# Performance work log

Hardware: AMD Instinct MI355X
Metric: run time of the kernel (lower is better)

The kernel has to match this reference:

```python
import jax, jax.numpy as jnp
import numpy as np

B, L, C = 4, 2048, 1024
H = 16
D = C // H  # head_dim = 64


def _rope(t, cos, sin):
    # t: [B, H, L, D]; cos/sin: [L, D//2] broadcast to [1, 1, L, D//2]
    te = t[..., ::2]
    to = t[..., 1::2]
    c = cos[None, None]
    s = sin[None, None]
    re = te * c - to * s
    ro = te * s + to * c
    # interleave even/odd back: [..., D//2, 2] -> [..., D]
    return jnp.stack([re, ro], axis=-1).reshape(t.shape)


def setup_inputs() -> dict:
    key = jax.random.key(0)
    ks = jax.random.split(key, 5)
    x = jax.random.normal(ks[0], (B, L, C), dtype=jnp.float32)
    # rotary phases: theta_i = 10000^(-2i/D), angles = pos * theta
    inv_freq = 1.0 / (10000.0 ** (np.arange(0, D, 2, dtype=np.float32) / D))
    ang = np.arange(L, dtype=np.float32)[:, None] * inv_freq[None, :]  # [L, D//2]
    cos = jnp.asarray(np.cos(ang))
    sin = jnp.asarray(np.sin(ang))
    w_qkv = jax.random.normal(ks[1], (3 * C, C), dtype=jnp.float32) * (C ** -0.5)
    w_proj = jax.random.normal(ks[2], (C, C), dtype=jnp.float32) * (C ** -0.5)
    b_proj = jnp.zeros((C,), dtype=jnp.float32)
    return {"x": x, "cos": cos, "sin": sin, "w_qkv": w_qkv, "w_proj": w_proj, "b_proj": b_proj}


def reference(x, cos, sin, w_qkv, w_proj, b_proj):
    Bx, Lx, Cx = x.shape
    # QKV projection (torch Linear: y = x @ W.T), then split heads
    qkv = jnp.einsum("blc,fc->blf", x, w_qkv)  # [B, L, 3C]
    qkv = qkv.reshape(Bx, Lx, 3, H, D).transpose(2, 0, 3, 1, 4)  # [3, B, H, L, D]
    q, k, v = qkv[0], qkv[1], qkv[2]
    q = _rope(q, cos, sin)
    k = _rope(k, cos, sin)
    # scaled dot-product attention, non-causal
    scale = D ** -0.5
    scores = jnp.einsum("bhqd,bhkd->bhqk", q, k) * scale
    attn = jax.nn.softmax(scores, axis=-1)
    o = jnp.einsum("bhqk,bhkd->bhqd", attn, v)  # [B, H, L, D]
    o = o.transpose(0, 2, 1, 3).reshape(Bx, Lx, Cx)
    return jnp.einsum("blc,fc->blf", o, w_proj) + b_proj
```

## Files before the change

kernel.cpp:

```cpp
#include <hip/hip_runtime.h>
#include <hip/hip_bf16.h>
#include <cstdint>


typedef unsigned short u16;
typedef __attribute__((ext_vector_type(8))) short bf16x8;
typedef __attribute__((ext_vector_type(4))) float f32x4;
typedef __attribute__((ext_vector_type(2))) unsigned int u32x2;

#define GLD16(g, l)                                                            \
  __builtin_amdgcn_global_load_lds(                                            \
      (const __attribute__((address_space(1))) void*)(g),                      \
      (__attribute__((address_space(3))) void*)(l), 16, 0, 0)

static __device__ __forceinline__ u16 f32_bf16(float f) {
  union { float f; unsigned u; } v; v.f = f;
  unsigned r = v.u + 0x7FFFu + ((v.u >> 16) & 1u);
  return (u16)(r >> 16);
}
static __device__ __forceinline__ float bf16_f32(u16 h) {
  union { unsigned u; float f; } v; v.u = ((unsigned)h) << 16;
  return v.f;
}
static __device__ __forceinline__ unsigned pack_rne(float a, float b) {
  union { float f; unsigned u; } x, y; x.f = a; y.f = b;
  unsigned ua = x.u + 0x7FFFu + ((x.u >> 16) & 1u);
  unsigned ub = y.u + 0x7FFFu + ((y.u >> 16) & 1u);
  return (ua >> 16) | (ub & 0xFFFF0000u);
}
static __device__ __forceinline__ unsigned pack_bf16_hw(float a, float b) {
  float2 t; t.x = a; t.y = b;
  __hip_bfloat162 h = __float22bfloat162_rn(t);
  union { __hip_bfloat162 h; unsigned u; } c; c.h = h;
  return c.u;
}
static __device__ __forceinline__ bf16x8 mk_pf(unsigned a, unsigned b,
                                               unsigned c, unsigned d) {
  union { unsigned u[4]; bf16x8 v; } t;
  t.u[0] = a; t.u[1] = b; t.u[2] = c; t.u[3] = d;
  return t.v;
}

__global__ __launch_bounds__(256) void convert_all(
    const void* __restrict__ x, const void* __restrict__ wq,
    const void* __restrict__ wp, const void* __restrict__ cs,
    const void* __restrict__ sn, const void* __restrict__ bs,
    u16* __restrict__ xb, u16* __restrict__ wqb, u16* __restrict__ wpb,
    u16* __restrict__ cb, u16* __restrict__ sb, u16* __restrict__ bb) {
  const unsigned f32mode = (((const unsigned*)cs)[0] == 0x3F800000u);
  int blk = blockIdx.x;
  const void* src; u16* dst; int i0, n4;
  if (blk < 8192)       { src = x;  dst = xb;  i0 = blk;         n4 = 2097152; }
  else if (blk < 11264) { src = wq; dst = wqb; i0 = blk - 8192;  n4 = 786432; }
  else if (blk < 12288) { src = wp; dst = wpb; i0 = blk - 11264; n4 = 262144; }
  else if (blk < 12352) { src = cs; dst = cb;  i0 = blk - 12288; n4 = 16384; }
  else if (blk < 12416) { src = sn; dst = sb;  i0 = blk - 12352; n4 = 16384; }
  else                  { src = bs; dst = bb;  i0 = blk - 12416; n4 = 256; }
  int i = i0 * 256 + threadIdx.x;
  if (i >= n4) return;
  if (f32mode) {
    float4 v = ((const float4*)src)[i];
    uint2 o;
    o.x = pack_rne(v.x, v.y);
    o.y = pack_rne(v.z, v.w);
    ((uint2*)dst)[i] = o;
  } else {
    ((uint2*)dst)[i] = ((const uint2*)src)[i];
  }
}

static __device__ __forceinline__ void gemm_mainloop(
    const u16* __restrict__ A, const u16* __restrict__ Bm, int K,
    int m0, int n0, u16* As, u16* Bs, f32x4 acc[4][4]) {
  const int tid  = threadIdx.x;
  const int lane = tid & 63;
  const int wave = tid >> 6;
  const int n16  = lane & 15;
  const int quad = lane >> 4;
  const int wm = (wave >> 1) * 64;
  const int wn = (wave & 1) * 64;
  const u16* ag = A  + (size_t)(m0 + wave * 16 + (lane >> 2)) * K + (lane & 3) * 8;
  const u16* bg = Bm + (size_t)(n0 + wave * 16 + (lane >> 2)) * K + (lane & 3) * 8;
  u16* al = As + wave * (16 * 32);
  u16* bl = Bs + wave * (16 * 32);
  for (int kt = 0; kt < K; kt += 32) {
    GLD16(ag + kt, al);
    GLD16(ag + (size_t)64 * K + kt, al + 64 * 32);
    GLD16(bg + kt, bl);
    GLD16(bg + (size_t)64 * K + kt, bl + 64 * 32);
    __syncthreads();
    bf16x8 af[4], bf[4];
#pragma unroll
    for (int i = 0; i < 4; i++)
      af[i] = *(const bf16x8*)(As + (wm + i * 16 + n16) * 32 + quad * 8);
#pragma unroll
    for (int j = 0; j < 4; j++)
      bf[j] = *(const bf16x8*)(Bs + (wn + j * 16 + n16) * 32 + quad * 8);
#pragma unroll
    for (int i = 0; i < 4; i++)
#pragma unroll
      for (int j = 0; j < 4; j++)
        acc[i][j] = __builtin_amdgcn_mfma_f32_16x16x32_bf16(af[i], bf[j], acc[i][j], 0, 0, 0);
    __syncthreads();
  }
}

__global__ __launch_bounds__(256) void gemm_qkv(
    const u16* __restrict__ x, const u16* __restrict__ w,
    u16* __restrict__ q_ws, u16* __restrict__ k_ws, u16* __restrict__ vt_ws) {
  __shared__ u16 As[128 * 32];
  __shared__ u16 Bs[128 * 32];
  f32x4 acc[4][4];
#pragma unroll
  for (int i = 0; i < 4; i++)
#pragma unroll
    for (int j = 0; j < 4; j++) acc[i][j] = (f32x4){0.f, 0.f, 0.f, 0.f};
  const int m0 = blockIdx.y * 128;
  const int n0 = blockIdx.x * 128;
  gemm_mainloop(x, w, 1024, m0, n0, As, Bs, acc);
  const int lane = threadIdx.x & 63, wave = threadIdx.x >> 6;
  const int n16 = lane & 15, quad = lane >> 4;
  const int wm = (wave >> 1) * 64, wn = (wave & 1) * 64;
#pragma unroll
  for (int i = 0; i < 4; i++)
#pragma unroll
    for (int j = 0; j < 4; j++) {
      int f = n0 + wn + j * 16 + n16;
      int which = f >> 10;
      int rem = f & 1023;
      int h = rem >> 6, d = rem & 63;
      int l0 = m0 + wm + i * 16 + quad * 4;
      int b = l0 >> 11, l = l0 & 2047;
      if (which == 2) {
        uint2 o;
        o.x = pack_rne(acc[i][j][0], acc[i][j][1]);
        o.y = pack_rne(acc[i][j][2], acc[i][j][3]);
        size_t idx = (((size_t)b * 16 + h) * 64 + d) * 2048 + l;
        *(uint2*)(vt_ws + idx) = o;
      } else {
        u16* dst = (which == 0) ? q_ws : k_ws;
        size_t base = (((size_t)b * 16 + h) * 2048 + l) * 64 + d;
#pragma unroll
        for (int r = 0; r < 4; r++)
          dst[base + (size_t)r * 64] = f32_bf16(acc[i][j][r]);
      }
    }
}

#define NP_ROPE 4194304
__global__ __launch_bounds__(256) void rope_qk(
    u16* __restrict__ q, u16* __restrict__ k,
    const u16* __restrict__ cosp, const u16* __restrict__ sinp) {
  int idx = blockIdx.x * 256 + threadIdx.x;
  bool isq = (idx < NP_ROPE);
  u16* t = isq ? q : k;
  float sc = isq ? 0.18033688011112042f : 1.0f;
  int p = isq ? idx : idx - NP_ROPE;
  int l = (p >> 5) & 2047;
  int i = p & 31;
  unsigned v = ((unsigned*)t)[p];
  float te = bf16_f32((u16)(v & 0xFFFFu));
  float to = bf16_f32((u16)(v >> 16));
  float c = bf16_f32(cosp[l * 32 + i]);
  float s = bf16_f32(sinp[l * 32 + i]);
  ((unsigned*)t)[p] = pack_rne((te * c - to * s) * sc, (te * s + to * c) * sc);
}

__global__ __launch_bounds__(256, 4) void flash_attn(
    const u16* __restrict__ q_ws, const u16* __restrict__ k_ws,
    const u16* __restrict__ vt_ws, u16* __restrict__ o_ws) {
  __shared__ u16 Ks[2][64 * 64];
  __shared__ u16 Vs[2][64 * 64];
  const int bh = blockIdx.x & 63;
  const int q0 = (blockIdx.x >> 6) * 128;
  const int b = bh >> 4, h = bh & 15;
  const int tid = threadIdx.x, lane = tid & 63, wave = tid >> 6;
  const int n16 = lane & 15, quad = lane >> 4;
  const int x7 = n16 & 7;
  const int pn16 = (n16 & 3) | ((n16 & 4) << 1) | ((n16 & 8) >> 1);
  const int px7 = pn16 & 7;
  const size_t hoff = (size_t)bh * (2048 * 64);

  bf16x8 qf[2][2];
#pragma unroll
  for (int qb = 0; qb < 2; qb++) {
    const u16* qrow = q_ws + hoff + (size_t)(q0 + wave * 32 + qb * 16 + n16) * 64;
    qf[qb][0] = *(const bf16x8*)(qrow + quad * 8);
    qf[qb][1] = *(const bf16x8*)(qrow + 32 + quad * 8);
  }

  f32x4 oacc[2][4];
  f32x4 lq[2];
#pragma unroll
  for (int qb = 0; qb < 2; qb++) {
    lq[qb] = (f32x4){0.f, 0.f, 0.f, 0.f};
#pragma unroll
    for (int s = 0; s < 4; s++) oacc[qb][s] = (f32x4){0.f, 0.f, 0.f, 0.f};
  }

  const int srow = wave * 8 + (lane >> 3);
  const int sw = (lane & 7) ^ ((lane >> 3) & 7);
  const u16* kg = k_ws + hoff + (size_t)srow * 64 + sw * 8;
  const u16* vg = vt_ws + hoff + (size_t)srow * 2048 + sw * 8;
  const int loff = wave * 8 * 64;

  GLD16(kg, &Ks[0][loff]);
  GLD16(kg + 32 * 64, &Ks[0][loff + 32 * 64]);
  GLD16(vg, &Vs[0][loff]);
  GLD16(vg + (size_t)32 * 2048, &Vs[0][loff + 32 * 64]);

  for (int kt = 0; kt < 2048; kt += 64) {
    const int buf = (kt >> 6) & 1;
    __syncthreads();
    if (kt + 64 < 2048) {
      const u16* kgn = kg + (size_t)(kt + 64) * 64;
      const u16* vgn = vg + (kt + 64);
      GLD16(kgn, &Ks[buf ^ 1][loff]);
      GLD16(kgn + 32 * 64, &Ks[buf ^ 1][loff + 32 * 64]);
      GLD16(vgn, &Vs[buf ^ 1][loff]);
      GLD16(vgn + (size_t)32 * 2048, &Vs[buf ^ 1][loff + 32 * 64]);
    }
    const u16* ks = Ks[buf];
    const u16* vs = Vs[buf];

    unsigned pxk[2][4], pyk[2][4];
#pragma unroll
    for (int sub = 0; sub < 4; sub++) {
      const u16* krow = ks + (sub * 16 + pn16) * 64;
      bf16x8 kf0 = *(const bf16x8*)(krow + (quad ^ px7) * 8);
      bf16x8 kf1 = *(const bf16x8*)(krow + ((quad + 4) ^ px7) * 8);
#pragma unroll
      for (int qb = 0; qb < 2; qb++) {
        f32x4 z = (f32x4){0.f, 0.f, 0.f, 0.f};
        z = __builtin_amdgcn_mfma_f32_16x16x32_bf16(kf0, qf[qb][0], z, 0, 0, 0);
        z = __builtin_amdgcn_mfma_f32_16x16x32_bf16(kf1, qf[qb][1], z, 0, 0, 0);
        f32x4 p;
#pragma unroll
        for (int r = 0; r < 4; r++) p[r] = __builtin_amdgcn_exp2f(z[r]);
        lq[qb] += p;
        pxk[qb][sub] = pack_bf16_hw(p[0], p[1]);
        pyk[qb][sub] = pack_bf16_hw(p[2], p[3]);
      }
    }

    bf16x8 pf[2][2];
#pragma unroll
    for (int qb = 0; qb < 2; qb++) {
      u32x2 r0 = __builtin_amdgcn_permlane32_swap(pxk[qb][0], pxk[qb][1], false, false);
      u32x2 r1 = __builtin_amdgcn_permlane32_swap(pyk[qb][0], pyk[qb][1], false, false);
      u32x2 r2 = __builtin_amdgcn_permlane32_swap(pxk[qb][2], pxk[qb][3], false, false);
      u32x2 r3 = __builtin_amdgcn_permlane32_swap(pyk[qb][2], pyk[qb][3], false, false);
      pf[qb][0] = mk_pf(r0.x, r1.x, r0.y, r1.y);
      pf[qb][1] = mk_pf(r2.x, r3.x, r2.y, r3.y);
    }

#pragma unroll
    for (int sd = 0; sd < 4; sd++) {
      const u16* vrow = vs + (sd * 16 + n16) * 64;
      bf16x8 vf0 = *(const bf16x8*)(vrow + (quad ^ x7) * 8);
      bf16x8 vf1 = *(const bf16x8*)(vrow + ((quad + 4) ^ x7) * 8);
#pragma unroll
      for (int qb = 0; qb < 2; qb++) {
        oacc[qb][sd] = __builtin_amdgcn_mfma_f32_16x16x32_bf16(pf[qb][0], vf0, oacc[qb][sd], 0, 0, 0);
        oacc[qb][sd] = __builtin_amdgcn_mfma_f32_16x16x32_bf16(pf[qb][1], vf1, oacc[qb][sd], 0, 0, 0);
      }
    }
  }

#pragma unroll
  for (int qb = 0; qb < 2; qb++) {
    float l = lq[qb][0] + lq[qb][1] + lq[qb][2] + lq[qb][3];
    l += __shfl_xor(l, 16, 64);
    l += __shfl_xor(l, 32, 64);
    float linv = 1.0f / l;
#pragma unroll
    for (int r = 0; r < 4; r++) {
      float lr = __shfl(linv, quad * 4 + r, 64);
      int row = q0 + wave * 32 + qb * 16 + quad * 4 + r;
      size_t base = ((size_t)b * 2048 + row) * 1024 + h * 64;
#pragma unroll
      for (int sd = 0; sd < 4; sd++)
        o_ws[base + sd * 16 + n16] = f32_bf16(oacc[qb][sd][r] * lr);
    }
  }
}

__global__ __launch_bounds__(256) void gemm_proj(
    const u16* __restrict__ o, const u16* __restrict__ w,
    const u16* __restrict__ bias, float* __restrict__ out) {
  __shared__ u16 As[128 * 32];
  __shared__ u16 Bs[128 * 32];
  f32x4 acc[4][4];
#pragma unroll
  for (int i = 0; i < 4; i++)
#pragma unroll
    for (int j = 0; j < 4; j++) acc[i][j] = (f32x4){0.f, 0.f, 0.f, 0.f};
  const int m0 = blockIdx.y * 128;
  const int n0 = blockIdx.x * 128;
  gemm_mainloop(o, w, 1024, m0, n0, As, Bs, acc);
  const int lane = threadIdx.x & 63, wave = threadIdx.x >> 6;
  const int n16 = lane & 15, quad = lane >> 4;
  const int wm = (wave >> 1) * 64, wn = (wave & 1) * 64;
#pragma unroll
  for (int i = 0; i < 4; i++)
#pragma unroll
    for (int j = 0; j < 4; j++) {
      int f = n0 + wn + j * 16 + n16;
      float bf = bf16_f32(bias[f]);
#pragma unroll
      for (int r = 0; r < 4; r++) {
        int m = m0 + wm + i * 16 + quad * 4 + r;
        out[(size_t)m * 1024 + f] = acc[i][j][r] + bf;
      }
    }
}

extern "C" void kernel_launch(void* const* d_in, const int* in_sizes, int n_in,
                              void* d_out, int out_size, void* d_ws, size_t ws_size,
                              hipStream_t stream) {
  float* out = (float*)d_out;

  u16* ws = (u16*)d_ws;
  u16* xb     = ws;
  u16* wqkvb  = ws + 8388608;
  u16* wprojb = ws + 11534336;
  u16* cosb   = ws + 12582912;
  u16* sinb   = ws + 12648448;
  u16* biasb  = ws + 12713984;
  u16* qb     = ws + 12715008;
  u16* kb     = ws + 21103616;
  u16* vtb    = ws + 29492224;
  u16* ob     = xb;

  convert_all<<<12417, 256, 0, stream>>>(
      d_in[0], d_in[3], d_in[4], d_in[1], d_in[2], d_in[5],
      xb, wqkvb, wprojb, cosb, sinb, biasb);

  gemm_qkv<<<dim3(24, 64), 256, 0, stream>>>(xb, wqkvb, qb, kb, vtb);
  rope_qk<<<32768, 256, 0, stream>>>(qb, kb, cosb, sinb);
  flash_attn<<<1024, 256, 0, stream>>>(qb, kb, vtb, ob);
  gemm_proj<<<dim3(8, 64), 256, 0, stream>>>(ob, wprojb, biasb, out);
}
```

Baseline: 288.0 us.

## Software-pipeline PV MFMAs one tile behind QK and add setprio around MFMA

Defers the P·V matrix multiply of each key tile into the next loop iteration, keeping the packed P fragments and V fragments in registers so the PV MFMAs overlap with the next tile's QK MFMAs and exp. A final drain after the loop handles the last tile. It also wraps the MFMA groups in s_setprio so waves issuing matrix ops get scheduling priority. This adds register pressure (V fragments held across the barrier), which may reduce occupancy.

```diff
diff --git a/kernel.cpp b/kernel.cpp
--- a/kernel.cpp
+++ b/kernel.cpp
@@ -209,6 +209,9 @@
   GLD16(vg, &Vs[0][loff]);
   GLD16(vg + (size_t)32 * 2048, &Vs[0][loff + 32 * 64]);
 
+  bf16x8 pfp[2][2];
+  bf16x8 vfp[4][2];
+
   for (int kt = 0; kt < 2048; kt += 64) {
     const int buf = (kt >> 6) & 1;
     __syncthreads();
@@ -232,8 +235,10 @@
 #pragma unroll
       for (int qb = 0; qb < 2; qb++) {
         f32x4 z = (f32x4){0.f, 0.f, 0.f, 0.f};
+        __builtin_amdgcn_s_setprio(1);
         z = __builtin_amdgcn_mfma_f32_16x16x32_bf16(kf0, qf[qb][0], z, 0, 0, 0);
         z = __builtin_amdgcn_mfma_f32_16x16x32_bf16(kf1, qf[qb][1], z, 0, 0, 0);
+        __builtin_amdgcn_s_setprio(0);
         f32x4 p;
 #pragma unroll
         for (int r = 0; r < 4; r++) p[r] = __builtin_amdgcn_exp2f(z[r]);
@@ -243,29 +248,45 @@
       }
     }
 
-    bf16x8 pf[2][2];
+    if (kt) {
+      __builtin_amdgcn_s_setprio(1);
+#pragma unroll
+      for (int sd = 0; sd < 4; sd++)
+#pragma unroll
+        for (int qb = 0; qb < 2; qb++) {
+          oacc[qb][sd] = __builtin_amdgcn_mfma_f32_16x16x32_bf16(pfp[qb][0], vfp[sd][0], oacc[qb][sd], 0, 0, 0);
+          oacc[qb][sd] = __builtin_amdgcn_mfma_f32_16x16x32_bf16(pfp[qb][1], vfp[sd][1], oacc[qb][sd], 0, 0, 0);
+        }
+      __builtin_amdgcn_s_setprio(0);
+    }
+
 #pragma unroll
     for (int qb = 0; qb < 2; qb++) {
       u32x2 r0 = __builtin_amdgcn_permlane32_swap(pxk[qb][0], pxk[qb][1], false, false);
       u32x2 r1 = __builtin_amdgcn_permlane32_swap(pyk[qb][0], pyk[qb][1], false, false);
       u32x2 r2 = __builtin_amdgcn_permlane32_swap(pxk[qb][2], pxk[qb][3], false, false);
       u32x2 r3 = __builtin_amdgcn_permlane32_swap(pyk[qb][2], pyk[qb][3], false, false);
-      pf[qb][0] = mk_pf(r0.x, r1.x, r0.y, r1.y);
-      pf[qb][1] = mk_pf(r2.x, r3.x, r2.y, r3.y);
+      pfp[qb][0] = mk_pf(r0.x, r1.x, r0.y, r1.y);
+      pfp[qb][1] = mk_pf(r2.x, r3.x, r2.y, r3.y);
     }
 
 #pragma unroll
     for (int sd = 0; sd < 4; sd++) {
       const u16* vrow = vs + (sd * 16 + n16) * 64;
-      bf16x8 vf0 = *(const bf16x8*)(vrow + (quad ^ x7) * 8);
-      bf16x8 vf1 = *(const bf16x8*)(vrow + ((quad + 4) ^ x7) * 8);
-#pragma unroll
-      for (int qb = 0; qb < 2; qb++) {
-        oacc[qb][sd] = __builtin_amdgcn_mfma_f32_16x16x32_bf16(pf[qb][0], vf0, oacc[qb][sd], 0, 0, 0);
-        oacc[qb][sd] = __builtin_amdgcn_mfma_f32_16x16x32_bf16(pf[qb][1], vf1, oacc[qb][sd], 0, 0, 0);
-      }
-    }
-  }
+      vfp[sd][0] = *(const bf16x8*)(vrow + (quad ^ x7) * 8);
+      vfp[sd][1] = *(const bf16x8*)(vrow + ((quad + 4) ^ x7) * 8);
+    }
+  }
+
+  __builtin_amdgcn_s_setprio(1);
+#pragma unroll
+  for (int sd = 0; sd < 4; sd++)
+#pragma unroll
+    for (int qb = 0; qb < 2; qb++) {
+      oacc[qb][sd] = __builtin_amdgcn_mfma_f32_16x16x32_bf16(pfp[qb][0], vfp[sd][0], oacc[qb][sd], 0, 0, 0);
+      oacc[qb][sd] = __builtin_amdgcn_mfma_f32_16x16x32_bf16(pfp[qb][1], vfp[sd][1], oacc[qb][sd], 0, 0, 0);
+    }
+  __builtin_amdgcn_s_setprio(0);
 
 #pragma unroll
   for (int qb = 0; qb < 2; qb++) {
```

New measurement: 386.4 us. 34.2% more time.
